# Kernel tuning notes

Hardware: AMD Instinct MI355X
Metric: run time of the kernel (lower is better)

## Reference

```python
import jax, jax.numpy as jnp
import numpy as np

C = 128        # in_channels == out_channels
KDIM = 16      # key/query dim k
UDIM = 1       # intra-depth u
HEADS = 4      # h
VDIM = C // HEADS  # v = 32
R = 3          # local context receptive field
EPS = 1e-5     # BatchNorm eps


def setup_inputs() -> dict:
    key = jax.random.key(0)
    ks = jax.random.split(key, 5)
    x = jax.random.normal(ks[0], (2, C, 48, 48, 48), jnp.float32)
    # 1x1x1 conv weights stored as [out_ch, in_ch] (matches nn.Conv3d kernel_size=1)
    Wq = jax.random.normal(ks[1], (KDIM * HEADS, C), jnp.float32) * (KDIM * C) ** (-0.5)
    Wk = jax.random.normal(ks[2], (KDIM * UDIM, C), jnp.float32) * C ** (-0.5)
    Wv = jax.random.normal(ks[3], (VDIM * UDIM, C), jnp.float32) * C ** (-0.5)
    # Conv4d weight (kdim, udim, 1, r, r, r) with kernel-depth 1 -> store as 3D conv kernel
    Wpos = jax.random.normal(ks[4], (KDIM, UDIM, R, R, R), jnp.float32) * 0.05
    gq = jnp.ones((KDIM * HEADS,), jnp.float32)
    bq = jnp.zeros((KDIM * HEADS,), jnp.float32)
    gv = jnp.ones((VDIM * UDIM,), jnp.float32)
    bv = jnp.zeros((VDIM * UDIM,), jnp.float32)
    return dict(x=x, Wq=Wq, Wk=Wk, Wv=Wv, Wpos=Wpos, gq=gq, bq=bq, gv=gv, bv=bv)


def _bn(t, g, b):
    # BatchNorm3d in training mode: batch statistics over (N, D, H, W)
    mean = t.mean(axis=(0, 2, 3, 4), keepdims=True)
    var = t.var(axis=(0, 2, 3, 4), keepdims=True)
    return (t - mean) * jax.lax.rsqrt(var + EPS) * g[None, :, None, None, None] + b[None, :, None, None, None]


def reference(x, Wq, Wk, Wv, Wpos, gq, bq, gv, bv):
    b, c, dd, hh, ww = x.shape
    n = dd * hh * ww
    # 1x1x1 convs as channel contractions
    q = _bn(jnp.einsum('oc,bcdhw->bodhw', Wq, x), gq, bq)
    k = jnp.einsum('oc,bcdhw->bodhw', Wk, x)
    v = _bn(jnp.einsum('oc,bcdhw->bodhw', Wv, x), gv, bv)
    q = q.reshape(b, HEADS, KDIM, n)          # b h k n
    k = k.reshape(b, UDIM, KDIM, n)           # b u k n
    vf = v.reshape(b, UDIM, VDIM, n)          # b u v n
    k = jax.nn.softmax(k, axis=-1)            # softmax over context positions
    # content lambda
    lam_c = jnp.einsum('bukm,buvm->bkv', k, vf)
    y_c = jnp.einsum('bhkn,bkv->bhvn', q, lam_c)
    # position lambda: Conv4d with kernel (1, r, r, r) over (v, d, h, w)
    # kernel-depth 1 along v == independent 3D conv on each v slice -> fold v into batch
    v6 = vf.reshape(b, UDIM, VDIM, dd, hh, ww)
    vconv = v6.transpose(0, 2, 1, 3, 4, 5).reshape(b * VDIM, UDIM, dd, hh, ww)
    p = R // 2
    lam_p = jax.lax.conv_general_dilated(
        vconv, Wpos, window_strides=(1, 1, 1), padding=[(p, p)] * 3,
        dimension_numbers=('NCDHW', 'OIDHW', 'NCDHW'))
    lam_p = lam_p.reshape(b, VDIM, KDIM, n)   # b v k n
    y_p = jnp.einsum('bhkn,bvkn->bhvn', q, lam_p)
    y = y_c + y_p                             # content=True and position=True
    return y.reshape(b, HEADS * VDIM, dd, hh, ww)
```

## Files before the change

### kernel.cpp

```cpp
#include <hip/hip_runtime.h>
#include <math.h>

#define NPOS 110592
#define EPS 1e-5f

using bf16x8 = __attribute__((ext_vector_type(8))) short;
using f32x4  = __attribute__((ext_vector_type(4))) float;
using f32x2  = __attribute__((ext_vector_type(2))) float;

constexpr long O_WB    = 0;
constexpr long O_WPT   = 7168;
constexpr long O_SARR  = 7600;
constexpr long O_TARR  = 7696;
constexpr long O_RMAX  = 7792;
constexpr long O_ZP    = 7824;
constexpr long O_RZI   = 14736;
constexpr long O_SW    = 14768;
constexpr long O_CW    = 16496;
constexpr long O_LAMC  = 16608;
constexpr long O_LAMC2 = 17632;
constexpr long O_BC    = 21728;
constexpr long O_LAMCP = 21984;
constexpr long O_Q     = 243168;
constexpr long O_K     = 7321056;
constexpr long O_V     = 10860000;

__device__ inline unsigned short f2bf(float f) {
    unsigned int u = __float_as_uint(f);
    u += 0x7FFFu + ((u >> 16) & 1u);
    return (unsigned short)(u >> 16);
}
__device__ inline float bflo(unsigned int u) { return __uint_as_float(u << 16); }
__device__ inline float bfhi(unsigned int u) { return __uint_as_float(u & 0xFFFF0000u); }
__device__ inline unsigned int cvtpk(float a, float b) {
    unsigned int r;
    asm("v_cvt_pk_bf16_f32 %0, %1, %2" : "=v"(r) : "v"(a), "v"(b));
    return r;
}
__device__ inline void pkfma(f32x2& c, f32x2 a, f32x2 b) {
    asm("v_pk_fma_f32 %0, %1, %2, %0" : "+v"(c) : "v"(a), "v"(b));
}

template<int CTRL>
__device__ inline float dpp_shr(float x) {
    int xi = __builtin_bit_cast(int, x);
    return __builtin_bit_cast(float, __builtin_amdgcn_update_dpp(xi, xi, CTRL, 0xf, 0xf, false));
}
__device__ inline float dpp_sum16(float x) {
    x += dpp_shr<0x111>(x);
    x += dpp_shr<0x112>(x);
    x += dpp_shr<0x114>(x);
    x += dpp_shr<0x118>(x);
    return x;
}
__device__ inline float dpp_max16(float x) {
    x = fmaxf(x, dpp_shr<0x111>(x));
    x = fmaxf(x, dpp_shr<0x112>(x));
    x = fmaxf(x, dpp_shr<0x114>(x));
    x = fmaxf(x, dpp_shr<0x118>(x));
    return x;
}

__global__ __launch_bounds__(256) void ksetup(const float* Wq, const float* Wk, const float* Wv,
                                              const float* Wpos, float* ws) {
    int i = blockIdx.x * 256 + threadIdx.x;
    if (i < 7168) {
        int oc = i >> 6, cp = i & 63;
        int c = 2 * cp;
        float v0, v1;
        if (oc < 64)      { v0 = Wq[oc * 128 + c];        v1 = Wq[oc * 128 + c + 1]; }
        else if (oc < 80) { v0 = Wk[(oc - 64) * 128 + c]; v1 = Wk[(oc - 64) * 128 + c + 1]; }
        else              { v0 = Wv[(oc - 80) * 128 + c]; v1 = Wv[(oc - 80) * 128 + c + 1]; }
        ((unsigned int*)(ws + O_WB))[i] = (unsigned int)f2bf(v0) | ((unsigned int)f2bf(v1) << 16);
    } else if (i < 7600) {
        int j = i - 7168;
        int o = j >> 4, k = j & 15;
        ws[O_WPT + j] = Wpos[k * 27 + o];
    }
}

__global__ __launch_bounds__(256, 4) void kproj(const float* __restrict__ x, const float* __restrict__ ws,
                                                unsigned int* __restrict__ qu, float* __restrict__ kr,
                                                unsigned int* __restrict__ vu,
                                                float* __restrict__ PS, float* __restrict__ PQ,
                                                float* __restrict__ PM) {
    __shared__ unsigned int xsu[64 * 68];
    __shared__ float pss[4 * 112], psq[4 * 112], pmx[4 * 16];
    const unsigned short* WBu = (const unsigned short*)(ws + O_WB);

    int blk0 = blockIdx.x;
    int blk = (blk0 & 7) * 432 + (blk0 >> 3);
    int b = blk / 1728, tile = blk - b * 1728;
    long base = (long)b * 128 * NPOS + (long)tile * 64;
    int tid = threadIdx.x;

    for (int i = tid; i < 64 * 64; i += 256) {
        int cp = i >> 6, p = i & 63;
        float v0 = x[base + (long)(2 * cp) * NPOS + p];
        float v1 = x[base + (long)(2 * cp + 1) * NPOS + p];
        xsu[p * 68 + cp] = cvtpk(v0, v1);
    }
    __syncthreads();

    int lane = tid & 63;
    int wv = __builtin_amdgcn_readfirstlane(tid >> 6);
    int r = lane & 15, g = lane >> 4;

    f32x4 acc[7];
#pragma unroll
    for (int t = 0; t < 7; ++t) acc[t] = (f32x4){0.f, 0.f, 0.f, 0.f};

    const unsigned short* xrow = (const unsigned short*)xsu + (wv * 16 + r) * 136;
#pragma unroll
    for (int ks = 0; ks < 4; ++ks) {
        bf16x8 bfrag = *(const bf16x8*)(const void*)(xrow + ks * 32 + g * 8);
#pragma unroll
        for (int t = 0; t < 7; ++t) {
            bf16x8 afrag = *(const bf16x8*)(const void*)(WBu + (t * 16 + r) * 128 + ks * 32 + g * 8);
            acc[t] = __builtin_amdgcn_mfma_f32_16x16x32_bf16(afrag, bfrag, acc[t], 0, 0, 0);
        }
    }

    long pos = (long)tile * 64 + wv * 16 + r;
#pragma unroll
    for (int t = 0; t < 4; ++t)
#pragma unroll
        for (int jp = 0; jp < 2; ++jp)
            qu[((long)b * 32 + t * 8 + g * 2 + jp) * NPOS + pos] = cvtpk(acc[t][2 * jp], acc[t][2 * jp + 1]);
#pragma unroll
    for (int j = 0; j < 4; ++j)
        kr[((long)b * 16 + g * 4 + j) * NPOS + pos] = acc[4][j];
#pragma unroll
    for (int t = 5; t < 7; ++t)
#pragma unroll
        for (int jp = 0; jp < 2; ++jp)
            vu[((long)b * 16 + (t - 5) * 8 + g * 2 + jp) * NPOS + pos] = cvtpk(acc[t][2 * jp], acc[t][2 * jp + 1]);

#pragma unroll
    for (int t = 0; t < 7; ++t) {
#pragma unroll
        for (int j = 0; j < 4; ++j) {
            float v = acc[t][j];
            float s = dpp_sum16(v);
            float q = dpp_sum16(v * v);
            if (r == 15) {
                int oc = t * 16 + g * 4 + j;
                pss[wv * 112 + oc] = s;
                psq[wv * 112 + oc] = q;
            }
        }
    }
#pragma unroll
    for (int j = 0; j < 4; ++j) {
        float m = dpp_max16(acc[4][j]);
        if (r == 15) pmx[wv * 16 + g * 4 + j] = m;
    }
    __syncthreads();
    if (tid < 112) {
        float s = pss[tid] + pss[112 + tid] + pss[224 + tid] + pss[336 + tid];
        float q = psq[tid] + psq[112 + tid] + psq[224 + tid] + psq[336 + tid];
        PS[(long)blk * 112 + tid] = s;
        PQ[(long)blk * 112 + tid] = q;
    } else if (tid < 128) {
        int kk = tid - 112;
        PM[(long)blk * 16 + kk] = fmaxf(fmaxf(pmx[kk], pmx[16 + kk]),
                                        fmaxf(pmx[32 + kk], pmx[48 + kk]));
    }
}

__global__ __launch_bounds__(256) void kred(const float* __restrict__ PS, const float* __restrict__ PQ,
                                            const float* __restrict__ PM,
                                            const float* gq, const float* bq,
                                            const float* gv, const float* bv, float* ws) {
    __shared__ float rs[256], rq[256];
    int bid = blockIdx.x, tid = threadIdx.x;
    if (bid < 96) {
        int c = bid;
        int oc = c < 64 ? c : c + 16;
        float s = 0.f, q = 0.f;
        for (int i = tid; i < 3456; i += 256) {
            s += PS[(long)i * 112 + oc];
            q += PQ[(long)i * 112 + oc];
        }
        rs[tid] = s; rq[tid] = q;
        __syncthreads();
        for (int st = 128; st > 0; st >>= 1) {
            if (tid < st) { rs[tid] += rs[tid + st]; rq[tid] += rq[tid + st]; }
            __syncthreads();
        }
        if (tid == 0) {
            const float inv_n = 1.f / 221184.f;
            float mean = rs[0] * inv_n;
            float var = rq[0] * inv_n - mean * mean;
            float g = c < 64 ? gq[c] : gv[c - 64];
            float bb = c < 64 ? bq[c] : bv[c - 64];
            float sc = g * rsqrtf(var + EPS);
            ws[O_SARR + c] = sc;
            ws[O_TARR + c] = bb - mean * sc;
        }
    } else {
        int row = bid - 96;
        int b = row >> 4, kk = row & 15;
        float m = -1e30f;
        for (int i = tid; i < 1728; i += 256) m = fmaxf(m, PM[((long)b * 1728 + i) * 16 + kk]);
        rs[tid] = m;
        __syncthreads();
        for (int st = 128; st > 0; st >>= 1) {
            if (tid < st) rs[tid] = fmaxf(rs[tid], rs[tid + st]);
            __syncthreads();
        }
        if (tid == 0) ws[O_RMAX + row] = rs[0];
    }
}

__global__ __launch_bounds__(256) void klamcp(const float* __restrict__ kr, const unsigned int* __restrict__ vu,
                                              float* __restrict__ ws, float* __restrict__ lamcp) {
    __shared__ float es[16 * 512];
    const float* rmax = ws + O_RMAX;
    int bid = blockIdx.x;
    int b = bid / 216, chunk = bid - b * 216;
    long p0 = (long)chunk * 512;
    int tid = threadIdx.x;
    for (int i = tid; i < 16 * 512; i += 256) {
        int rr = i >> 9, p = i & 511;
        es[i] = expf(kr[((long)b * 16 + rr) * NPOS + p0 + p] - rmax[b * 16 + rr]);
    }
    __syncthreads();
    int vp = tid >> 4, pl = tid & 15;
    const unsigned int* vpp = vu + ((long)b * 16 + vp) * NPOS + p0;
    float acc0[16], acc1[16];
#pragma unroll
    for (int k = 0; k < 16; ++k) { acc0[k] = 0.f; acc1[k] = 0.f; }
    for (int j = 0; j < 32; ++j) {
        int p = pl + 16 * j;
        unsigned int u = vpp[p];
        float v0 = bflo(u), v1 = bfhi(u);
#pragma unroll
        for (int k = 0; k < 16; ++k) {
            float e = es[k * 512 + p];
            acc0[k] = fmaf(e, v0, acc0[k]);
            acc1[k] = fmaf(e, v1, acc1[k]);
        }
    }
#pragma unroll
    for (int m = 1; m < 16; m <<= 1) {
#pragma unroll
        for (int k = 0; k < 16; ++k) {
            acc0[k] += __shfl_xor(acc0[k], m, 64);
            acc1[k] += __shfl_xor(acc1[k], m, 64);
        }
    }
    if (pl == 0) {
        long base = (long)bid * 512;
#pragma unroll
        for (int k = 0; k < 16; ++k) {
            lamcp[base + k * 32 + 2 * vp]     = acc0[k];
            lamcp[base + k * 32 + 2 * vp + 1] = acc1[k];
        }
    }
    {
        int rr = tid >> 4, j = tid & 15;
        float s = 0.f;
        const float* er = es + rr * 512 + j * 32;
#pragma unroll 8
        for (int i = 0; i < 32; ++i) s += er[i];
#pragma unroll
        for (int m = 1; m < 16; m <<= 1) s += __shfl_xor(s, m, 64);
        if (j == 0) ws[O_ZP + (long)bid * 16 + rr] = s;
    }
}

__global__ __launch_bounds__(256) void kfin2(float* ws) {
    int tid = threadIdx.x;
    if (tid < 32) {
        int b = tid >> 4, kk = tid & 15;
        float s = 0.f;
        for (int c = 0; c < 216; ++c) s += ws[O_ZP + ((long)b * 216 + c) * 16 + kk];
        ws[O_RZI + tid] = 1.f / s;
    }
    for (int i = tid; i < 1728; i += 256) {
        int h = i / 432, r = i - h * 432, o = r >> 4, k = r & 15;
        ws[O_SW + i] = ws[O_SARR + h * 16 + k] * ws[O_WPT + o * 16 + k];
    }
    if (tid < 108) {
        int h = tid / 27, o = tid - h * 27;
        float s = 0.f;
        for (int k = 0; k < 16; ++k) s += ws[O_TARR + h * 16 + k] * ws[O_WPT + o * 16 + k];
        ws[O_CW + tid] = s;
    }
}

__global__ __launch_bounds__(256) void klamcred(float* ws) {
    int out = blockIdx.x * 256 + threadIdx.x;
    if (out >= 1024) return;
    int b = out >> 9, idx = out & 511;
    int kk = idx >> 5, v = idx & 31;
    const float* lamcp = ws + O_LAMCP;
    float S = 0.f;
    for (int c = 0; c < 216; ++c) S += lamcp[((long)b * 216 + c) * 512 + idx];
    float sv = ws[O_SARR + 64 + v], tv = ws[O_TARR + 64 + v];
    ws[O_LAMC + out] = sv * S * ws[O_RZI + b * 16 + kk] + tv;
}

__global__ __launch_bounds__(256) void klamc3(float* ws) {
    int tid = threadIdx.x;
    for (int i = tid; i < 4096; i += 256) {
        int b = i >> 11, r = i & 2047;
        int h = r >> 9, k = (r >> 5) & 15, v = r & 31;
        ws[O_LAMC2 + i] = ws[O_SARR + h * 16 + k] * ws[O_LAMC + b * 512 + k * 32 + v];
    }
    {
        int i = tid;
        int b = i >> 7, h = (i >> 5) & 3, v = i & 31;
        float s = 0.f;
#pragma unroll
        for (int k = 0; k < 16; ++k) s += ws[O_TARR + h * 16 + k] * ws[O_LAMC + b * 512 + k * 32 + v];
        ws[O_BC + i] = s;
    }
}

__global__ __launch_bounds__(512, 4) void kfinal(const unsigned int* __restrict__ qu,
                                                 const unsigned int* __restrict__ vu,
                                                 const float* __restrict__ ws, float* __restrict__ y) {
    __shared__ unsigned int vbnu[432 * 16];
    __shared__ unsigned short qwh[27 * 128 * 4];
    __shared__ unsigned int qsu[128 * 32];
    const float* sarr  = ws + O_SARR;
    const float* tarr  = ws + O_TARR;
    const float* swp   = ws + O_SW;
    const float* cwp   = ws + O_CW;
    const float* lamc2 = ws + O_LAMC2;
    const float* bcp   = ws + O_BC;

    int bid0 = blockIdx.x;
    int bid = (bid0 & 7) * 216 + (bid0 >> 3);
    int b = bid / 864, t = bid - b * 864;
    int td = t / 36, r = t - td * 36;
    int th = r / 3, tw = r - th * 3;
    int d0 = td * 2, h0 = th * 4, w0 = tw * 16;
    int tid = threadIdx.x;

    for (int i = tid; i < 16 * 432; i += 512) {
        int vp = i / 432, z = i - vp * 432;
        int zd = z / 108, rr = z - zd * 108;
        int zh = rr / 18, zw = rr - zh * 18;
        int gd = d0 - 1 + zd, gh = h0 - 1 + zh, gw = w0 - 1 + zw;
        unsigned int out = 0u;
        if ((unsigned)gd < 48u && (unsigned)gh < 48u && (unsigned)gw < 48u) {
            unsigned int u = vu[((long)b * 16 + vp) * NPOS + gd * 2304 + gh * 48 + gw];
            float a = fmaf(bflo(u), sarr[64 + 2 * vp], tarr[64 + 2 * vp]);
            float c = fmaf(bfhi(u), sarr[65 + 2 * vp], tarr[65 + 2 * vp]);
            out = cvtpk(a, c);
        }
        int sl = (vp >> 2) ^ ((z ^ (z >> 2)) & 3);
        vbnu[z * 16 + sl * 4 + (vp & 3)] = out;
    }

    int lane = tid & 63;
    int wv = __builtin_amdgcn_readfirstlane(tid >> 6);
    int hsel = wv & 3, psel = wv >> 2;
    int pos_l = psel * 64 + lane;
    int lh = lane >> 4, lw = lane & 15;
    int goff = (d0 + psel) * 2304 + (h0 + lh) * 48 + (w0 + lw);
    {
        unsigned int uq[8];
        float qk[16];
        const unsigned int* qb = qu + ((long)b * 32 + hsel * 8) * NPOS + goff;
#pragma unroll
        for (int m = 0; m < 8; ++m) {
            uq[m] = qb[(long)m * NPOS];
            qk[2 * m] = bflo(uq[m]);
            qk[2 * m + 1] = bfhi(uq[m]);
        }
#pragma unroll
        for (int o = 0; o < 27; ++o) {
            float a = cwp[hsel * 27 + o];
            const float* swrow = swp + (hsel * 27 + o) * 16;
#pragma unroll
            for (int k = 0; k < 16; ++k) a = fmaf(qk[k], swrow[k], a);
            qwh[(o * 128 + pos_l) * 4 + hsel] = (unsigned short)cvtpk(a, a);
        }
        uint4 w0v = make_uint4(uq[0], uq[1], uq[2], uq[3]);
        uint4 w1v = make_uint4(uq[4], uq[5], uq[6], uq[7]);
        *(uint4*)(qsu + pos_l * 32 + (((2 * hsel) ^ (pos_l & 7)) << 2)) = w0v;
        *(uint4*)(qsu + pos_l * 32 + (((2 * hsel + 1) ^ (pos_l & 7)) << 2)) = w1v;
    }
    __syncthreads();

    int vg = wv & 3;
    int v0 = vg * 8;
    f32x2 acc2[4][4];
#pragma unroll
    for (int hh = 0; hh < 4; ++hh)
#pragma unroll
        for (int p = 0; p < 4; ++p) {
            acc2[hh][p][0] = bcp[(b * 4 + hh) * 32 + v0 + 2 * p];
            acc2[hh][p][1] = bcp[(b * 4 + hh) * 32 + v0 + 2 * p + 1];
        }

#pragma unroll
    for (int s = 0; s < 8; ++s) {
        uint4 uq = *(const uint4*)(qsu + pos_l * 32 + ((s ^ (pos_l & 7)) << 2));
        int hh = s >> 1, k0 = (s & 1) * 8;
        float qa[8];
        qa[0] = bflo(uq.x); qa[1] = bfhi(uq.x);
        qa[2] = bflo(uq.y); qa[3] = bfhi(uq.y);
        qa[4] = bflo(uq.z); qa[5] = bfhi(uq.z);
        qa[6] = bflo(uq.w); qa[7] = bfhi(uq.w);
#pragma unroll
        for (int j = 0; j < 8; ++j) {
            const float* l2 = lamc2 + (((b * 4 + hh) * 16 + k0 + j) << 5) + v0;
#pragma unroll
            for (int p = 0; p < 4; ++p) {
                acc2[hh][p][0] = fmaf(qa[j], l2[2 * p], acc2[hh][p][0]);
                acc2[hh][p][1] = fmaf(qa[j], l2[2 * p + 1], acc2[hh][p][1]);
            }
        }
    }

    int zb = psel * 108 + lh * 18 + lw;
#pragma unroll
    for (int od = 0; od < 3; ++od)
#pragma unroll
    for (int oh = 0; oh < 3; ++oh)
#pragma unroll
    for (int ow = 0; ow < 3; ++ow) {
        int o = od * 9 + oh * 3 + ow;
        int z = zb + od * 108 + oh * 18 + ow;
        int sl = vg ^ ((z ^ (z >> 2)) & 3);
        uint4 u = *(const uint4*)(vbnu + z * 16 + (sl << 2));
        uint2 uqw = *(const uint2*)(qwh + ((o * 128 + pos_l) << 2));
        f32x2 s0; s0[0] = bflo(u.x); s0[1] = bfhi(u.x);
        f32x2 s1; s1[0] = bflo(u.y); s1[1] = bfhi(u.y);
        f32x2 s2; s2[0] = bflo(u.z); s2[1] = bfhi(u.z);
        f32x2 s3; s3[0] = bflo(u.w); s3[1] = bfhi(u.w);
        float q0 = bflo(uqw.x), q1 = bfhi(uqw.x);
        float q2 = bflo(uqw.y), q3 = bfhi(uqw.y);
        f32x2 qd0; qd0[0] = q0; qd0[1] = q0;
        f32x2 qd1; qd1[0] = q1; qd1[1] = q1;
        f32x2 qd2; qd2[0] = q2; qd2[1] = q2;
        f32x2 qd3; qd3[0] = q3; qd3[1] = q3;
        pkfma(acc2[0][0], qd0, s0); pkfma(acc2[0][1], qd0, s1);
        pkfma(acc2[0][2], qd0, s2); pkfma(acc2[0][3], qd0, s3);
        pkfma(acc2[1][0], qd1, s0); pkfma(acc2[1][1], qd1, s1);
        pkfma(acc2[1][2], qd1, s2); pkfma(acc2[1][3], qd1, s3);
        pkfma(acc2[2][0], qd2, s0); pkfma(acc2[2][1], qd2, s1);
        pkfma(acc2[2][2], qd2, s2); pkfma(acc2[2][3], qd2, s3);
        pkfma(acc2[3][0], qd3, s0); pkfma(acc2[3][1], qd3, s1);
        pkfma(acc2[3][2], qd3, s2); pkfma(acc2[3][3], qd3, s3);
    }

    long pbase = (long)b * 128 * NPOS + goff;
#pragma unroll
    for (int hh = 0; hh < 4; ++hh)
#pragma unroll
        for (int p = 0; p < 4; ++p) {
            y[pbase + (long)(hh * 32 + v0 + 2 * p) * NPOS]     = acc2[hh][p][0];
            y[pbase + (long)(hh * 32 + v0 + 2 * p + 1) * NPOS] = acc2[hh][p][1];
        }
}

extern "C" void kernel_launch(void* const* d_in, const int* in_sizes, int n_in,
                              void* d_out, int out_size, void* d_ws, size_t ws_size,
                              hipStream_t stream) {
    const float* x    = (const float*)d_in[0];
    const float* Wq   = (const float*)d_in[1];
    const float* Wk   = (const float*)d_in[2];
    const float* Wv   = (const float*)d_in[3];
    const float* Wpos = (const float*)d_in[4];
    const float* gq   = (const float*)d_in[5];
    const float* bq   = (const float*)d_in[6];
    const float* gv   = (const float*)d_in[7];
    const float* bv   = (const float*)d_in[8];
    float* ws = (float*)d_ws;
    float* y  = (float*)d_out;
    unsigned int* qu = (unsigned int*)(ws + O_Q);
    float*        kr = ws + O_K;
    unsigned int* vu = (unsigned int*)(ws + O_V);
    float* PS = y;
    float* PQ = y + 387072;
    float* PM = y + 774144;

    ksetup  <<<30,   256, 0, stream>>>(Wq, Wk, Wv, Wpos, ws);
    kproj   <<<3456, 256, 0, stream>>>(x, ws, qu, kr, vu, PS, PQ, PM);
    kred    <<<128,  256, 0, stream>>>(PS, PQ, PM, gq, bq, gv, bv, ws);
    klamcp  <<<432,  256, 0, stream>>>(kr, vu, ws, ws + O_LAMCP);
    kfin2   <<<1,    256, 0, stream>>>(ws);
    klamcred<<<4,    256, 0, stream>>>(ws);
    klamc3  <<<1,    256, 0, stream>>>(ws);
    kfinal  <<<1728, 512, 0, stream>>>(qu, vu, ws, y);
}
```

Baseline: 221.7 us.

## Fuse lambda reduction kernels, widen x loads, use packed FMA in final

Three small tail kernels (kfin2, klamcred, klamc3) are merged into one two-block kfold kernel that keeps the reduced content lambda in shared memory, removing two launches and a global round trip. kproj's input staging now has each thread convert eight channels and write one 16-byte word to LDS instead of 4-byte stores. kfinal's content-lambda accumulation uses packed two-wide FMAs over float2 loads. The fused kernel does its serial 216-step reduction with only two blocks, so per-thread latency on that path may still dominate.

```diff
diff --git a/kernel.cpp b/kernel.cpp
--- a/kernel.cpp
+++ b/kernel.cpp
@@ -94,11 +94,15 @@
     long base = (long)b * 128 * NPOS + (long)tile * 64;
     int tid = threadIdx.x;
 
-    for (int i = tid; i < 64 * 64; i += 256) {
-        int cp = i >> 6, p = i & 63;
-        float v0 = x[base + (long)(2 * cp) * NPOS + p];
-        float v1 = x[base + (long)(2 * cp + 1) * NPOS + p];
-        xsu[p * 68 + cp] = cvtpk(v0, v1);
+    for (int i = tid; i < 1024; i += 256) {
+        int cc = i >> 6, p = i & 63;
+        const float* xp = x + base + (long)(8 * cc) * NPOS + p;
+        uint4 w;
+        w.x = cvtpk(xp[0],               xp[(long)NPOS]);
+        w.y = cvtpk(xp[2 * (long)NPOS],  xp[3 * (long)NPOS]);
+        w.z = cvtpk(xp[4 * (long)NPOS],  xp[5 * (long)NPOS]);
+        w.w = cvtpk(xp[6 * (long)NPOS],  xp[7 * (long)NPOS]);
+        *(uint4*)(xsu + p * 68 + cc * 4) = w;
     }
     __syncthreads();
 
@@ -270,52 +274,50 @@
     }
 }
 
-__global__ __launch_bounds__(256) void kfin2(float* ws) {
-    int tid = threadIdx.x;
-    if (tid < 32) {
-        int b = tid >> 4, kk = tid & 15;
+__global__ __launch_bounds__(512) void kfold(float* ws) {
+    __shared__ float lamlds[512];
+    int b = blockIdx.x, tid = threadIdx.x;
+    const float* lamcp = ws + O_LAMCP;
+
+    float S = 0.f;
+    for (int c = 0; c < 216; ++c) S += lamcp[((long)b * 216 + c) * 512 + tid];
+
+    if (tid < 16) {
+        float z = 0.f;
+        for (int c = 0; c < 216; ++c) z += ws[O_ZP + ((long)b * 216 + c) * 16 + tid];
+        ws[O_RZI + b * 16 + tid] = 1.f / z;
+    }
+    if (b == 0) {
+        for (int i = tid; i < 1728; i += 512) {
+            int h = i / 432, r = i - h * 432, o = r >> 4, k = r & 15;
+            ws[O_SW + i] = ws[O_SARR + h * 16 + k] * ws[O_WPT + o * 16 + k];
+        }
+        if (tid < 108) {
+            int h = tid / 27, o = tid - h * 27;
+            float s = 0.f;
+            for (int k = 0; k < 16; ++k) s += ws[O_TARR + h * 16 + k] * ws[O_WPT + o * 16 + k];
+            ws[O_CW + tid] = s;
+        }
+    }
+    __syncthreads();
+
+    {
+        int kk = tid >> 5, v = tid & 31;
+        float sv = ws[O_SARR + 64 + v], tv = ws[O_TARR + 64 + v];
+        lamlds[tid] = sv * S * ws[O_RZI + b * 16 + kk] + tv;
+    }
+    __syncthreads();
+
+    for (int r = tid; r < 2048; r += 512) {
+        int h = r >> 9, k = (r >> 5) & 15;
+        ws[O_LAMC2 + (long)b * 2048 + r] = ws[O_SARR + h * 16 + k] * lamlds[r & 511];
+    }
+    if (tid < 128) {
+        int h = tid >> 5, v = tid & 31;
         float s = 0.f;
-        for (int c = 0; c < 216; ++c) s += ws[O_ZP + ((long)b * 216 + c) * 16 + kk];
-        ws[O_RZI + tid] = 1.f / s;
-    }
-    for (int i = tid; i < 1728; i += 256) {
-        int h = i / 432, r = i - h * 432, o = r >> 4, k = r & 15;
-        ws[O_SW + i] = ws[O_SARR + h * 16 + k] * ws[O_WPT + o * 16 + k];
-    }
-    if (tid < 108) {
-        int h = tid / 27, o = tid - h * 27;
-        float s = 0.f;
-        for (int k = 0; k < 16; ++k) s += ws[O_TARR + h * 16 + k] * ws[O_WPT + o * 16 + k];
-        ws[O_CW + tid] = s;
-    }
-}
-
-__global__ __launch_bounds__(256) void klamcred(float* ws) {
-    int out = blockIdx.x * 256 + threadIdx.x;
-    if (out >= 1024) return;
-    int b = out >> 9, idx = out & 511;
-    int kk = idx >> 5, v = idx & 31;
-    const float* lamcp = ws + O_LAMCP;
-    float S = 0.f;
-    for (int c = 0; c < 216; ++c) S += lamcp[((long)b * 216 + c) * 512 + idx];
-    float sv = ws[O_SARR + 64 + v], tv = ws[O_TARR + 64 + v];
-    ws[O_LAMC + out] = sv * S * ws[O_RZI + b * 16 + kk] + tv;
-}
-
-__global__ __launch_bounds__(256) void klamc3(float* ws) {
-    int tid = threadIdx.x;
-    for (int i = tid; i < 4096; i += 256) {
-        int b = i >> 11, r = i & 2047;
-        int h = r >> 9, k = (r >> 5) & 15, v = r & 31;
-        ws[O_LAMC2 + i] = ws[O_SARR + h * 16 + k] * ws[O_LAMC + b * 512 + k * 32 + v];
-    }
-    {
-        int i = tid;
-        int b = i >> 7, h = (i >> 5) & 3, v = i & 31;
-        float s = 0.f;
-#pragma unroll
-        for (int k = 0; k < 16; ++k) s += ws[O_TARR + h * 16 + k] * ws[O_LAMC + b * 512 + k * 32 + v];
-        ws[O_BC + i] = s;
+#pragma unroll
+        for (int k = 0; k < 16; ++k) s += ws[O_TARR + h * 16 + k] * lamlds[k * 32 + v];
+        ws[O_BC + b * 128 + tid] = s;
     }
 }
 
@@ -409,12 +411,12 @@
         qa[6] = bflo(uq.w); qa[7] = bfhi(uq.w);
 #pragma unroll
         for (int j = 0; j < 8; ++j) {
-            const float* l2 = lamc2 + (((b * 4 + hh) * 16 + k0 + j) << 5) + v0;
-#pragma unroll
-            for (int p = 0; p < 4; ++p) {
-                acc2[hh][p][0] = fmaf(qa[j], l2[2 * p], acc2[hh][p][0]);
-                acc2[hh][p][1] = fmaf(qa[j], l2[2 * p + 1], acc2[hh][p][1]);
-            }
+            const f32x2* l2 = (const f32x2*)(lamc2 + (((b * 4 + hh) * 16 + k0 + j) << 5) + v0);
+            f32x2 qd; qd[0] = qa[j]; qd[1] = qa[j];
+            pkfma(acc2[hh][0], qd, l2[0]);
+            pkfma(acc2[hh][1], qd, l2[1]);
+            pkfma(acc2[hh][2], qd, l2[2]);
+            pkfma(acc2[hh][3], qd, l2[3]);
         }
     }
 
@@ -481,12 +483,10 @@
     float* PQ = y + 387072;
     float* PM = y + 774144;
 
-    ksetup  <<<30,   256, 0, stream>>>(Wq, Wk, Wv, Wpos, ws);
-    kproj   <<<3456, 256, 0, stream>>>(x, ws, qu, kr, vu, PS, PQ, PM);
-    kred    <<<128,  256, 0, stream>>>(PS, PQ, PM, gq, bq, gv, bv, ws);
-    klamcp  <<<432,  256, 0, stream>>>(kr, vu, ws, ws + O_LAMCP);
-    kfin2   <<<1,    256, 0, stream>>>(ws);
-    klamcred<<<4,    256, 0, stream>>>(ws);
-    klamc3  <<<1,    256, 0, stream>>>(ws);
-    kfinal  <<<1728, 512, 0, stream>>>(qu, vu, ws, y);
-}
+    ksetup <<<30,   256, 0, stream>>>(Wq, Wk, Wv, Wpos, ws);
+    kproj  <<<3456, 256, 0, stream>>>(x, ws, qu, kr, vu, PS, PQ, PM);
+    kred   <<<128,  256, 0, stream>>>(PS, PQ, PM, gq, bq, gv, bv, ws);
+    klamcp <<<432,  256, 0, stream>>>(kr, vu, ws, ws + O_LAMCP);
+    kfold  <<<2,    512, 0, stream>>>(ws);
+    kfinal <<<1728, 512, 0, stream>>>(qu, vu, ws, y);
+}
```

Result: no change. 225.1 us (+1.5%).
